# Optimization experiments

Hardware: AMD Instinct MI355X
Metric: run time of the kernel (lower is better)

The kernel has to match this reference:

```python
import jax, jax.numpy as jnp
import numpy as np

B, T, D, H = 128, 512, 1024, 1024


def setup_inputs() -> dict:
    key = jax.random.key(0)
    ks = jax.random.split(key, 9)
    s = 1.0 / np.sqrt(D + H)
    return {
        "inputs": jax.random.normal(ks[0], (B, T, D), dtype=jnp.float32),
        "Wf": jax.random.normal(ks[1], (D + H, H), dtype=jnp.float32) * s,
        "bf": jax.random.normal(ks[2], (H,), dtype=jnp.float32) * s,
        "Wi": jax.random.normal(ks[3], (D + H, H), dtype=jnp.float32) * s,
        "bi": jax.random.normal(ks[4], (H,), dtype=jnp.float32) * s,
        "Wo": jax.random.normal(ks[5], (D + H, H), dtype=jnp.float32) * s,
        "bo": jax.random.normal(ks[6], (H,), dtype=jnp.float32) * s,
        "Wc": jax.random.normal(ks[7], (D + H, H), dtype=jnp.float32) * s,
        "bc": jax.random.normal(ks[8], (H,), dtype=jnp.float32) * s,
    }


def reference(inputs, Wf, bf, Wi, bi, Wo, bo, Wc, bc):
    # inputs: [B, T, D]; gates computed from concat(x_t, h_t) @ W + b.
    # Fuse the 4 gate Linears into one GEMM (same math, single contraction).
    batch = inputs.shape[0]
    hid = Wf.shape[1]
    W = jnp.concatenate([Wf, Wi, Wo, Wc], axis=1)          # [D+H, 4H]
    b = jnp.concatenate([bf, bi, bo, bc])                   # [4H]

    def step(carry, x_t):
        h, c = carry
        z = jnp.concatenate([x_t, h], axis=1) @ W + b        # [B, 4H]
        f, i, o, g = jnp.split(z, 4, axis=1)
        f = jax.nn.sigmoid(f)
        i = jax.nn.sigmoid(i)
        o = jax.nn.sigmoid(o)
        g = jnp.tanh(g)
        c = f * c + i * g
        h = o * jnp.tanh(c)
        return (h, c), h

    h0 = jnp.zeros((batch, hid), dtype=inputs.dtype)
    c0 = jnp.zeros((batch, hid), dtype=inputs.dtype)
    _, hs = jax.lax.scan(step, (h0, c0), jnp.swapaxes(inputs, 0, 1))  # hs: [T, B, H]
    # Original prepends each new hidden state -> outputs are in REVERSE time order.
    return jnp.flip(jnp.swapaxes(hs, 0, 1), axis=1)          # [B, T, H]
```

## Files before the change

### kernel.cpp

```cpp
#include <hip/hip_runtime.h>
#include <hip/hip_bf16.h>

#define Bb 128
#define Tt 512
#define Dd 1024
#define Hh 1024
#define KD 2048
#define CCH 32
#define NCHUNK (Tt / CCH)
#define NBLK 256

typedef __attribute__((ext_vector_type(4))) float f32x4;
typedef __attribute__((ext_vector_type(8))) short s16x8;
typedef __attribute__((address_space(1))) const void gcvoid;
typedef __attribute__((address_space(3))) void lvoid;

__device__ __forceinline__ unsigned short f2bf(float f) {
    union { float f; unsigned u; } v;
    v.f = f;
    unsigned r = v.u + 0x7fffu + ((v.u >> 16) & 1u);
    return (unsigned short)(r >> 16);
}

__device__ __forceinline__ s16x8 cvt8(const float* src) {
    f32x4 a = *reinterpret_cast<const f32x4*>(src);
    f32x4 b = *reinterpret_cast<const f32x4*>(src + 4);
    s16x8 v;
    v[0] = (short)f2bf(a[0]); v[1] = (short)f2bf(a[1]);
    v[2] = (short)f2bf(a[2]); v[3] = (short)f2bf(a[3]);
    v[4] = (short)f2bf(b[0]); v[5] = (short)f2bf(b[1]);
    v[6] = (short)f2bf(b[2]); v[7] = (short)f2bf(b[3]);
    return v;
}

__device__ __forceinline__ float sigf(float x)      { return 1.f / (1.f + __expf(-x)); }
__device__ __forceinline__ float tanhfast(float x)  { return 1.f - 2.f / (1.f + __expf(2.f * x)); }

__device__ __forceinline__ void cload16(s16x8* dst, const unsigned short* p) {
    asm volatile("global_load_dwordx4 %0, %1, off sc1"
                 : "=v"(*dst) : "v"(p) : "memory");
}
__device__ __forceinline__ void cstore2(unsigned short* p, unsigned v) {
    asm volatile("global_store_short %0, %1, off sc1" :: "v"(p), "v"(v) : "memory");
}

__device__ __forceinline__ void gbar(unsigned* cntA, unsigned* cntB,
                                     unsigned* flag, int t, int bid) {
    asm volatile("s_waitcnt vmcnt(0)" ::: "memory");
    __syncthreads();
    if (threadIdx.x == 0) {
        unsigned* ca = cntA + ((size_t)t * 8 + (bid & 7)) * 32;
        unsigned o = __hip_atomic_fetch_add(ca, 1u, __ATOMIC_RELAXED, __HIP_MEMORY_SCOPE_AGENT);
        if (o == 31u) {
            unsigned* cb = cntB + (size_t)t * 32;
            unsigned o2 = __hip_atomic_fetch_add(cb, 1u, __ATOMIC_RELAXED, __HIP_MEMORY_SCOPE_AGENT);
            if (o2 == 7u)
                __hip_atomic_store(flag + t, 1u, __ATOMIC_RELAXED, __HIP_MEMORY_SCOPE_AGENT);
        }
        while (__hip_atomic_load(flag + t, __ATOMIC_RELAXED, __HIP_MEMORY_SCOPE_AGENT) == 0u)
            __builtin_amdgcn_s_sleep(1);
    }
    __syncthreads();
}

__global__ __launch_bounds__(256) void zx_gemm(
    const float* __restrict__ X, const unsigned short* __restrict__ Wr,
    const float* __restrict__ bre, float* __restrict__ Zxc, int t0)
{
    __shared__ __align__(16) unsigned short ALds[2][128 * 64];
    __shared__ __align__(16) unsigned short BLds[2][128 * 64];

    const int tid = threadIdx.x, lane = tid & 63, wv = tid >> 6;
    const int wr = wv >> 1, wc = wv & 1;
    const int m0 = (blockIdx.x >> 5) * 128, n0 = (blockIdx.x & 31) * 128;

    f32x4 acc[4][4];
#pragma unroll
    for (int i = 0; i < 4; ++i)
#pragma unroll
        for (int jn = 0; jn < 4; ++jn) acc[i][jn] = 0.f;

    auto stage = [&](int buf, int ki) {
        const int k0 = ki * 64;
#pragma unroll
        for (int i = 0; i < 4; ++i) {
            int slot = i * 256 + tid;
            int r = slot >> 3, cp = slot & 7;
            int c = cp ^ (r & 7);
            int m = m0 + r, b = m >> 5, tc = m & 31;
            const float* src = X + ((size_t)b * Tt + t0 + tc) * Dd + k0 + c * 8;
            *reinterpret_cast<s16x8*>(&ALds[buf][slot * 8]) = cvt8(src);
        }
#pragma unroll
        for (int i = 0; i < 4; ++i) {
            int slot = i * 256 + tid;
            int r = slot >> 3, cp = slot & 7;
            int c = cp ^ (r & 7);
            const unsigned short* src = Wr + (size_t)(n0 + r) * KD + k0 + c * 8;
            *reinterpret_cast<s16x8*>(&BLds[buf][slot * 8]) =
                *reinterpret_cast<const s16x8*>(src);
        }
    };

    auto compute = [&](int buf) {
#pragma unroll
        for (int ks = 0; ks < 2; ++ks) {
            int ck = ks * 4 + (lane >> 4);
            s16x8 af[4], bf8[4];
#pragma unroll
            for (int m = 0; m < 4; ++m) {
                int ra = wr * 64 + m * 16 + (lane & 15);
                af[m] = *reinterpret_cast<const s16x8*>(&ALds[buf][ra * 64 + (ck ^ (ra & 7)) * 8]);
            }
#pragma unroll
            for (int n = 0; n < 4; ++n) {
                int rb = wc * 64 + n * 16 + (lane & 15);
                bf8[n] = *reinterpret_cast<const s16x8*>(&BLds[buf][rb * 64 + (ck ^ (rb & 7)) * 8]);
            }
#pragma unroll
            for (int m = 0; m < 4; ++m)
#pragma unroll
                for (int n = 0; n < 4; ++n)
                    acc[m][n] = __builtin_amdgcn_mfma_f32_16x16x32_bf16(af[m], bf8[n], acc[m][n], 0, 0, 0);
        }
    };

    stage(0, 0);
#pragma unroll 1
    for (int ki = 0; ki < 16; ++ki) {
        __syncthreads();
        if (ki + 1 < 16) stage((ki + 1) & 1, ki + 1);
        compute(ki & 1);
    }

#pragma unroll
    for (int ni = 0; ni < 4; ++ni) {
        int gcol = n0 + wc * 64 + ni * 16 + (lane & 15);
        float bias = bre[gcol];
        int gg = gcol >> 5, nn = gcol & 31;
        int zcol = gg * 32 + (nn & 7) * 4 + (nn >> 3);
#pragma unroll
        for (int mi = 0; mi < 4; ++mi) {
            int rbase = m0 + wr * 64 + mi * 16 + (lane >> 4) * 4;
#pragma unroll
            for (int r = 0; r < 4; ++r)
                Zxc[(size_t)(rbase + r) * 4096 + zcol] = acc[mi][ni][r] + bias;
        }
    }
}

__global__ __launch_bounds__(256) void lstm_chunk(
    const unsigned short* __restrict__ Wr,
    const float* __restrict__ Zxc,
    unsigned short* __restrict__ hbuf,
    float* __restrict__ cbuf,
    float* __restrict__ out,
    unsigned* __restrict__ cntA,
    unsigned* __restrict__ cntB,
    unsigned* __restrict__ flag,
    int t0)
{
    __shared__ __align__(16) unsigned short Bl[32 * 1024];

    const int tid = threadIdx.x, lane = tid & 63, w = tid >> 6;
    const int bid = blockIdx.x;
    const int g = bid >> 1, mh = bid & 1;

#pragma unroll
    for (int i = 0; i < 16; ++i) {
        int q = (w * 16 + i) * 64 + lane;
        int n = q >> 7, cp = q & 127;
        int cs = (cp & ~7) | ((cp ^ n) & 7);
        const unsigned short* src = Wr + (size_t)(g * 32 + n) * KD + Dd + cs * 8;
        __builtin_amdgcn_global_load_lds((gcvoid*)src,
            (lvoid*)&Bl[(w * 16 + i) * 512], 16, 0, 0);
    }
    asm volatile("s_waitcnt vmcnt(0)" ::: "memory");
    __syncthreads();

    const int r0 = mh * 64 + w * 16 + (lane & 15);
    const int nlo = lane & 15;
    const unsigned short* b0p = &Bl[nlo * 1024];
    const int jj = lane & 7, j = g * 8 + jj;
    const bool hi = (lane & 8) != 0;
    const int rowb = mh * 64 + w * 16 + (lane >> 4) * 4;

    f32x4 creg;
#pragma unroll
    for (int r = 0; r < 4; ++r)
        creg[r] = cbuf[(size_t)(rowb + r) * Hh + j];

    f32x4 zx[4];
#pragma unroll
    for (int r = 0; r < 4; ++r)
        zx[r] = *reinterpret_cast<const f32x4*>(
            Zxc + ((size_t)(rowb + r) * CCH + 0) * 4096 + j * 4);

#pragma unroll 1
    for (int tt = 0; tt < CCH; ++tt) {
        const int t = t0 + tt;
        const unsigned short* hin = hbuf + (size_t)(t & 1) * (Bb * Hh);
        unsigned short* houtp = hbuf + (size_t)((t + 1) & 1) * (Bb * Hh);
        const unsigned short* arow = hin + (size_t)r0 * Hh + (lane >> 4) * 8;

        f32x4 acc0 = 0.f, acc1 = 0.f;

        s16x8 afb[2][8];
#pragma unroll
        for (int i = 0; i < 8; ++i)
            cload16(&afb[0][i], arow + i * 32);

#pragma unroll
        for (int b = 0; b < 4; ++b) {
            if (b < 3) {
#pragma unroll
                for (int i = 0; i < 8; ++i)
                    cload16(&afb[(b + 1) & 1][i], arow + ((b + 1) * 8 + i) * 32);
                asm volatile("s_waitcnt vmcnt(8)" ::: "memory");
            } else {
                asm volatile("s_waitcnt vmcnt(0)" ::: "memory");
            }
            __builtin_amdgcn_sched_barrier(0);
#pragma unroll
            for (int i = 0; i < 8; ++i) {
                int ki = b * 8 + i;
                int ck = ki * 4 + (lane >> 4);
                int p = (ck & ~7) | ((ck ^ nlo) & 7);
                s16x8 b0 = *reinterpret_cast<const s16x8*>(b0p + p * 8);
                s16x8 b1 = *reinterpret_cast<const s16x8*>(b0p + 16 * 1024 + p * 8);
                acc0 = __builtin_amdgcn_mfma_f32_16x16x32_bf16(afb[b & 1][i], b0, acc0, 0, 0, 0);
                acc1 = __builtin_amdgcn_mfma_f32_16x16x32_bf16(afb[b & 1][i], b1, acc1, 0, 0, 0);
            }
        }

        f32x4 y0, y1;
#pragma unroll
        for (int r = 0; r < 4; ++r) {
            y0[r] = __shfl_xor(acc0[r], 8, 64);
            y1[r] = __shfl_xor(acc1[r], 8, 64);
        }

        f32x4 zxn[4];
        if (tt + 1 < CCH) {
#pragma unroll
            for (int r = 0; r < 4; ++r)
                zxn[r] = *reinterpret_cast<const f32x4*>(
                    Zxc + ((size_t)(rowb + r) * CCH + (tt + 1)) * 4096 + j * 4);
        }

#pragma unroll
        for (int r = 0; r < 4; ++r) {
            float vf = hi ? y0[r] : acc0[r];
            float vi = hi ? acc0[r] : y0[r];
            float vo = hi ? y1[r] : acc1[r];
            float vg = hi ? acc1[r] : y1[r];
            float zf = vf + zx[r][0], zi = vi + zx[r][1];
            float zo = vo + zx[r][2], zc = vg + zx[r][3];
            float fg = sigf(zf), ig = sigf(zi), og = sigf(zo), gv = tanhfast(zc);
            float cnew = fg * creg[r] + ig * gv;
            creg[r] = cnew;
            float hn = og * tanhfast(cnew);
            int row = rowb + r;
            cstore2(houtp + (size_t)row * Hh + j, (unsigned)f2bf(hn));
            out[((size_t)row * Tt + (Tt - 1 - t)) * Hh + j] = hn;
        }
#pragma unroll
        for (int r = 0; r < 4; ++r) zx[r] = zxn[r];

        if (tt + 1 < CCH) gbar(cntA, cntB, flag, t, bid);
    }

#pragma unroll
    for (int r = 0; r < 4; ++r)
        cbuf[(size_t)(rowb + r) * Hh + j] = creg[r];
}

__global__ __launch_bounds__(256) void conv_w(
    const float* __restrict__ Wf, const float* __restrict__ Wi,
    const float* __restrict__ Wo, const float* __restrict__ Wc,
    unsigned short* __restrict__ Wr)
{
    __shared__ float sm[64 * 65];
    const int tid = threadIdx.x;
    const int bid = blockIdx.x;
    const int gate = bid & 3;
    const int rest = bid >> 2;
    const int k0 = (rest & 31) * 64;
    const int c0 = (rest >> 5) * 64;
    const float* Wg = (gate == 0) ? Wf : (gate == 1) ? Wi : (gate == 2) ? Wo : Wc;

#pragma unroll
    for (int it = 0; it < 16; ++it) {
        int kl = it * 4 + (tid >> 6), cl = tid & 63;
        sm[kl * 65 + cl] = Wg[(size_t)(k0 + kl) * Hh + c0 + cl];
    }
    __syncthreads();
#pragma unroll
    for (int it = 0; it < 16; ++it) {
        int nl = it * 4 + (tid >> 6), kl = tid & 63;
        int col = c0 + nl;
        int n = (col >> 3) * 32 + gate * 8 + (col & 7);
        Wr[(size_t)n * KD + k0 + kl] = f2bf(sm[kl * 65 + nl]);
    }
}

#define NBAR_U32 (512 * 8 * 32 + 512 * 32 + 512)

__global__ void init_all(unsigned short* __restrict__ hbuf, float* __restrict__ cbuf,
                         unsigned* __restrict__ bars, float* __restrict__ bre,
                         const float* __restrict__ bF, const float* __restrict__ bI,
                         const float* __restrict__ bO, const float* __restrict__ bC) {
    int i = blockIdx.x * 256 + threadIdx.x;
    if (i < 2 * Bb * Hh) hbuf[i] = 0;
    if (i < Bb * Hh) cbuf[i] = 0.f;
    if (i < NBAR_U32) bars[i] = 0u;
    if (i < 4096) {
        int gate = (i >> 3) & 3, g = i >> 5, jjv = i & 7;
        int col = g * 8 + jjv;
        const float* bg = (gate == 0) ? bF : (gate == 1) ? bI : (gate == 2) ? bO : bC;
        bre[i] = bg[col];
    }
}

__global__ __launch_bounds__(256) void lstm_step(
    const float* __restrict__ X, const unsigned short* __restrict__ Wr,
    const float* __restrict__ bre,
    const unsigned short* __restrict__ hin, unsigned short* __restrict__ hout,
    float* __restrict__ cbuf, float* __restrict__ out, int t)
{
    __shared__ __align__(16) unsigned short Alds[2][64 * 64];
    __shared__ __align__(16) unsigned short Blds[2][32 * 64];
    __shared__ float zlds[64 * 33];

    const int tid = threadIdx.x, lane = tid & 63, w = tid >> 6;
    const int g = blockIdx.x >> 1, mh = blockIdx.x & 1;

    f32x4 acc[2];
    acc[0] = 0.f; acc[1] = 0.f;

    auto stageA = [&](int buf, int ki) {
        const int k0 = ki * 64;
#pragma unroll
        for (int i = 0; i < 2; ++i) {
            int slot = tid + 256 * i;
            int r = slot >> 3, cp = slot & 7;
            int c = cp ^ (r & 7);
            int k = k0 + c * 8;
            s16x8 v;
            if (k < Dd) {
                v = cvt8(X + ((size_t)(mh * 64 + r) * Tt + t) * Dd + k);
            } else {
                v = *reinterpret_cast<const s16x8*>(hin + (size_t)(mh * 64 + r) * Hh + (k - Dd));
            }
            *reinterpret_cast<s16x8*>(&Alds[buf][slot * 8]) = v;
        }
    };
    auto stageB = [&](int buf, int ki) {
        int n = tid >> 3, cp = tid & 7;
        int c = cp ^ (n & 7);
        const unsigned short* src = Wr + (size_t)(g * 32 + n) * KD + ki * 64 + c * 8;
        *reinterpret_cast<s16x8*>(&Blds[buf][tid * 8]) = *reinterpret_cast<const s16x8*>(src);
    };
    auto compute = [&](int buf) {
#pragma unroll
        for (int ks = 0; ks < 2; ++ks) {
            int ra = w * 16 + (lane & 15);
            int cha = (ks * 4 + (lane >> 4)) ^ (ra & 7);
            s16x8 af = *reinterpret_cast<const s16x8*>(&Alds[buf][ra * 64 + cha * 8]);
#pragma unroll
            for (int nt = 0; nt < 2; ++nt) {
                int n = nt * 16 + (lane & 15);
                int chb = (ks * 4 + (lane >> 4)) ^ (n & 7);
                s16x8 bf8 = *reinterpret_cast<const s16x8*>(&Blds[buf][n * 64 + chb * 8]);
                acc[nt] = __builtin_amdgcn_mfma_f32_16x16x32_bf16(af, bf8, acc[nt], 0, 0, 0);
            }
        }
    };

    stageA(0, 0); stageB(0, 0);
#pragma unroll 1
    for (int ki = 0; ki < 32; ++ki) {
        __syncthreads();
        if (ki + 1 < 32) { stageA((ki + 1) & 1, ki + 1); stageB((ki + 1) & 1, ki + 1); }
        compute(ki & 1);
    }

    {
        int rbase = w * 16 + (lane >> 4) * 4;
#pragma unroll
        for (int nt = 0; nt < 2; ++nt) {
            int col = nt * 16 + (lane & 15);
#pragma unroll
            for (int r = 0; r < 4; ++r)
                zlds[(rbase + r) * 33 + col] = acc[nt][r];
        }
    }
    __syncthreads();

#pragma unroll
    for (int it = 0; it < 2; ++it) {
        int idx = tid + it * 256;
        int row = idx >> 3, jj = idx & 7;
        int jx = g * 8 + jj;
        int grow = mh * 64 + row;
        float zf = zlds[row * 33 + jj]      + bre[g * 32 + jj];
        float zi = zlds[row * 33 + 8 + jj]  + bre[g * 32 + 8 + jj];
        float zo = zlds[row * 33 + 16 + jj] + bre[g * 32 + 16 + jj];
        float zc = zlds[row * 33 + 24 + jj] + bre[g * 32 + 24 + jj];
        float fg = sigf(zf), ig = sigf(zi), og = sigf(zo), gv = tanhfast(zc);
        float cold = cbuf[(size_t)grow * Hh + jx];
        float cnew = fg * cold + ig * gv;
        cbuf[(size_t)grow * Hh + jx] = cnew;
        float hn = og * tanhfast(cnew);
        hout[(size_t)grow * Hh + jx] = f2bf(hn);
        out[((size_t)grow * Tt + (Tt - 1 - t)) * Hh + jx] = hn;
    }
}

extern "C" void kernel_launch(void* const* d_in, const int* in_sizes, int n_in,
                              void* d_out, int out_size, void* d_ws, size_t ws_size,
                              hipStream_t stream) {
    (void)in_sizes; (void)n_in; (void)out_size;
    const float* X  = (const float*)d_in[0];
    const float* Wf = (const float*)d_in[1];
    const float* bF = (const float*)d_in[2];
    const float* Wi = (const float*)d_in[3];
    const float* bI = (const float*)d_in[4];
    const float* Wo = (const float*)d_in[5];
    const float* bO = (const float*)d_in[6];
    const float* Wc = (const float*)d_in[7];
    const float* bC = (const float*)d_in[8];
    float* out = (float*)d_out;

    char* ws = (char*)d_ws;
    size_t off = 0;
    auto carve = [&](size_t sz) { char* p = ws + off; off = (off + sz + 255) & ~(size_t)255; return p; };
    unsigned short* Wr   = (unsigned short*)carve((size_t)4096 * KD * 2);
    float*          bre  = (float*)carve(4096 * 4);
    unsigned short* hbuf = (unsigned short*)carve((size_t)2 * Bb * Hh * 2);
    float*          cbuf = (float*)carve((size_t)Bb * Hh * 4);
    unsigned*       bars = (unsigned*)carve((size_t)NBAR_U32 * 4);
    float*          Zxc  = (float*)carve((size_t)4096 * 4096 * 4);
    const size_t need = off;

    unsigned* cntA = bars;
    unsigned* cntB = bars + 512 * 8 * 32;
    unsigned* flag = bars + 512 * 8 * 32 + 512 * 32;

    conv_w<<<2048, 256, 0, stream>>>(Wf, Wi, Wo, Wc, Wr);
    init_all<<<1024, 256, 0, stream>>>(hbuf, cbuf, bars, bre, bF, bI, bO, bC);

    if (ws_size >= need) {
        const unsigned short* Wr_c = Wr;
        const float* Zxc_c = Zxc;
        for (int c = 0; c < NCHUNK; ++c) {
            int t0 = c * CCH;
            zx_gemm<<<1024, 256, 0, stream>>>(X, Wr, bre, Zxc, t0);
            void* args[] = {(void*)&Wr_c, (void*)&Zxc_c, (void*)&hbuf, (void*)&cbuf,
                            (void*)&out, (void*)&cntA, (void*)&cntB, (void*)&flag, (void*)&t0};
            hipLaunchCooperativeKernel((void*)lstm_chunk, dim3(NBLK), dim3(256), args, 0, stream);
        }
    } else {
        for (int t = 0; t < Tt; ++t) {
            const unsigned short* hin = hbuf + (size_t)(t & 1) * Bb * Hh;
            unsigned short*      houtp = hbuf + (size_t)((t + 1) & 1) * Bb * Hh;
            lstm_step<<<256, 256, 0, stream>>>(X, Wr, bre, hin, houtp, cbuf, out, t);
        }
    }
}
```

Measured before the change: 5.402 ms.

## Halve recurrent blocks to 128, widen per-block hidden slice, use flag-array grid barrier

The recurrent chunk kernel now runs 128 cooperative blocks instead of 256. Each block owns 16 hidden units across all 4 gates and keeps a 128KB LDS slice of the recurrent weights, so all four gate accumulators sit in registers and the cross-lane shuffles go away. The weight, bias and Zx column layouts are remapped to match. The two-level atomic counter barrier is replaced by per-block flag stores that one wavefront polls with vector loads, which is meant to cut barrier latency per timestep. In exchange each block does twice the MFMA work per step, so fewer CUs are active, and it depends on 128KB of LDS per block fitting.

Result: slower. 6.139 ms (+13.6%).

```diff
diff --git a/kernel.cpp b/kernel.cpp
--- a/kernel.cpp
+++ b/kernel.cpp
@@ -8,10 +8,11 @@
 #define KD 2048
 #define CCH 32
 #define NCHUNK (Tt / CCH)
-#define NBLK 256
+#define NBLK 128
 
 typedef __attribute__((ext_vector_type(4))) float f32x4;
 typedef __attribute__((ext_vector_type(8))) short s16x8;
+typedef __attribute__((ext_vector_type(4))) unsigned u32x4;
 typedef __attribute__((address_space(1))) const void gcvoid;
 typedef __attribute__((address_space(3))) void lvoid;
 
@@ -44,21 +45,23 @@
     asm volatile("global_store_short %0, %1, off sc1" :: "v"(p), "v"(v) : "memory");
 }
 
-__device__ __forceinline__ void gbar(unsigned* cntA, unsigned* cntB,
-                                     unsigned* flag, int t, int bid) {
+__device__ __forceinline__ void gbar(unsigned* flags, int t, int bid) {
     asm volatile("s_waitcnt vmcnt(0)" ::: "memory");
     __syncthreads();
-    if (threadIdx.x == 0) {
-        unsigned* ca = cntA + ((size_t)t * 8 + (bid & 7)) * 32;
-        unsigned o = __hip_atomic_fetch_add(ca, 1u, __ATOMIC_RELAXED, __HIP_MEMORY_SCOPE_AGENT);
-        if (o == 31u) {
-            unsigned* cb = cntB + (size_t)t * 32;
-            unsigned o2 = __hip_atomic_fetch_add(cb, 1u, __ATOMIC_RELAXED, __HIP_MEMORY_SCOPE_AGENT);
-            if (o2 == 7u)
-                __hip_atomic_store(flag + t, 1u, __ATOMIC_RELAXED, __HIP_MEMORY_SCOPE_AGENT);
-        }
-        while (__hip_atomic_load(flag + t, __ATOMIC_RELAXED, __HIP_MEMORY_SCOPE_AGENT) == 0u)
+    if (threadIdx.x < 64) {
+        unsigned* base = flags + (size_t)t * NBLK;
+        if (threadIdx.x == 0)
+            asm volatile("global_store_dword %0, %1, off sc1"
+                         :: "v"(base + bid), "v"(1u) : "memory");
+        const unsigned* sp = base + (threadIdx.x & 31) * 4;
+        for (;;) {
+            u32x4 f;
+            asm volatile("global_load_dwordx4 %0, %1, off sc1"
+                         : "=v"(f) : "v"(sp) : "memory");
+            asm volatile("s_waitcnt vmcnt(0)" ::: "memory");
+            if (__all((f[0] & f[1] & f[2] & f[3]) != 0u)) break;
             __builtin_amdgcn_s_sleep(1);
+        }
     }
     __syncthreads();
 }
@@ -137,8 +140,8 @@
     for (int ni = 0; ni < 4; ++ni) {
         int gcol = n0 + wc * 64 + ni * 16 + (lane & 15);
         float bias = bre[gcol];
-        int gg = gcol >> 5, nn = gcol & 31;
-        int zcol = gg * 32 + (nn & 7) * 4 + (nn >> 3);
+        int g = gcol >> 6, rem = gcol & 63, gate = rem >> 4, jj = rem & 15;
+        int zcol = (g * 16 + jj) * 4 + gate;
 #pragma unroll
         for (int mi = 0; mi < 4; ++mi) {
             int rbase = m0 + wr * 64 + mi * 16 + (lane >> 4) * 4;
@@ -155,34 +158,31 @@
     unsigned short* __restrict__ hbuf,
     float* __restrict__ cbuf,
     float* __restrict__ out,
-    unsigned* __restrict__ cntA,
-    unsigned* __restrict__ cntB,
-    unsigned* __restrict__ flag,
+    unsigned* __restrict__ flags,
     int t0)
 {
-    __shared__ __align__(16) unsigned short Bl[32 * 1024];
+    __shared__ __align__(16) unsigned short Bl[64 * 1024];
 
     const int tid = threadIdx.x, lane = tid & 63, w = tid >> 6;
     const int bid = blockIdx.x;
     const int g = bid >> 1, mh = bid & 1;
 
 #pragma unroll
-    for (int i = 0; i < 16; ++i) {
-        int q = (w * 16 + i) * 64 + lane;
+    for (int i = 0; i < 32; ++i) {
+        int q = (w * 32 + i) * 64 + lane;
         int n = q >> 7, cp = q & 127;
         int cs = (cp & ~7) | ((cp ^ n) & 7);
-        const unsigned short* src = Wr + (size_t)(g * 32 + n) * KD + Dd + cs * 8;
+        const unsigned short* src = Wr + (size_t)(g * 64 + n) * KD + Dd + cs * 8;
         __builtin_amdgcn_global_load_lds((gcvoid*)src,
-            (lvoid*)&Bl[(w * 16 + i) * 512], 16, 0, 0);
+            (lvoid*)&Bl[(w * 32 + i) * 512], 16, 0, 0);
     }
     asm volatile("s_waitcnt vmcnt(0)" ::: "memory");
     __syncthreads();
 
-    const int r0 = mh * 64 + w * 16 + (lane & 15);
     const int nlo = lane & 15;
+    const int r0 = mh * 64 + w * 16 + nlo;
     const unsigned short* b0p = &Bl[nlo * 1024];
-    const int jj = lane & 7, j = g * 8 + jj;
-    const bool hi = (lane & 8) != 0;
+    const int j = g * 16 + nlo;
     const int rowb = mh * 64 + w * 16 + (lane >> 4) * 4;
 
     f32x4 creg;
@@ -203,7 +203,9 @@
         unsigned short* houtp = hbuf + (size_t)((t + 1) & 1) * (Bb * Hh);
         const unsigned short* arow = hin + (size_t)r0 * Hh + (lane >> 4) * 8;
 
-        f32x4 acc0 = 0.f, acc1 = 0.f;
+        f32x4 acc[4];
+#pragma unroll
+        for (int n = 0; n < 4; ++n) acc[n] = 0.f;
 
         s16x8 afb[2][8];
 #pragma unroll
@@ -226,18 +228,12 @@
                 int ki = b * 8 + i;
                 int ck = ki * 4 + (lane >> 4);
                 int p = (ck & ~7) | ((ck ^ nlo) & 7);
-                s16x8 b0 = *reinterpret_cast<const s16x8*>(b0p + p * 8);
-                s16x8 b1 = *reinterpret_cast<const s16x8*>(b0p + 16 * 1024 + p * 8);
-                acc0 = __builtin_amdgcn_mfma_f32_16x16x32_bf16(afb[b & 1][i], b0, acc0, 0, 0, 0);
-                acc1 = __builtin_amdgcn_mfma_f32_16x16x32_bf16(afb[b & 1][i], b1, acc1, 0, 0, 0);
-            }
-        }
-
-        f32x4 y0, y1;
-#pragma unroll
-        for (int r = 0; r < 4; ++r) {
-            y0[r] = __shfl_xor(acc0[r], 8, 64);
-            y1[r] = __shfl_xor(acc1[r], 8, 64);
+#pragma unroll
+                for (int n = 0; n < 4; ++n) {
+                    s16x8 bf8 = *reinterpret_cast<const s16x8*>(b0p + n * 16384 + p * 8);
+                    acc[n] = __builtin_amdgcn_mfma_f32_16x16x32_bf16(afb[b & 1][i], bf8, acc[n], 0, 0, 0);
+                }
+            }
         }
 
         f32x4 zxn[4];
@@ -250,12 +246,10 @@
 
 #pragma unroll
         for (int r = 0; r < 4; ++r) {
-            float vf = hi ? y0[r] : acc0[r];
-            float vi = hi ? acc0[r] : y0[r];
-            float vo = hi ? y1[r] : acc1[r];
-            float vg = hi ? acc1[r] : y1[r];
-            float zf = vf + zx[r][0], zi = vi + zx[r][1];
-            float zo = vo + zx[r][2], zc = vg + zx[r][3];
+            float zf = acc[0][r] + zx[r][0];
+            float zi = acc[1][r] + zx[r][1];
+            float zo = acc[2][r] + zx[r][2];
+            float zc = acc[3][r] + zx[r][3];
             float fg = sigf(zf), ig = sigf(zi), og = sigf(zo), gv = tanhfast(zc);
             float cnew = fg * creg[r] + ig * gv;
             creg[r] = cnew;
@@ -267,7 +261,7 @@
 #pragma unroll
         for (int r = 0; r < 4; ++r) zx[r] = zxn[r];
 
-        if (tt + 1 < CCH) gbar(cntA, cntB, flag, t, bid);
+        if (tt + 1 < CCH) gbar(flags, t, bid);
     }
 
 #pragma unroll
@@ -299,24 +293,55 @@
     for (int it = 0; it < 16; ++it) {
         int nl = it * 4 + (tid >> 6), kl = tid & 63;
         int col = c0 + nl;
+        int n = (col >> 4) * 64 + gate * 16 + (col & 15);
+        Wr[(size_t)n * KD + k0 + kl] = f2bf(sm[kl * 65 + nl]);
+    }
+}
+
+__global__ __launch_bounds__(256) void conv_w_old(
+    const float* __restrict__ Wf, const float* __restrict__ Wi,
+    const float* __restrict__ Wo, const float* __restrict__ Wc,
+    unsigned short* __restrict__ Wr)
+{
+    __shared__ float sm[64 * 65];
+    const int tid = threadIdx.x;
+    const int bid = blockIdx.x;
+    const int gate = bid & 3;
+    const int rest = bid >> 2;
+    const int k0 = (rest & 31) * 64;
+    const int c0 = (rest >> 5) * 64;
+    const float* Wg = (gate == 0) ? Wf : (gate == 1) ? Wi : (gate == 2) ? Wo : Wc;
+
+#pragma unroll
+    for (int it = 0; it < 16; ++it) {
+        int kl = it * 4 + (tid >> 6), cl = tid & 63;
+        sm[kl * 65 + cl] = Wg[(size_t)(k0 + kl) * Hh + c0 + cl];
+    }
+    __syncthreads();
+#pragma unroll
+    for (int it = 0; it < 16; ++it) {
+        int nl = it * 4 + (tid >> 6), kl = tid & 63;
+        int col = c0 + nl;
         int n = (col >> 3) * 32 + gate * 8 + (col & 7);
         Wr[(size_t)n * KD + k0 + kl] = f2bf(sm[kl * 65 + nl]);
     }
 }
 
-#define NBAR_U32 (512 * 8 * 32 + 512 * 32 + 512)
+#define NBAR_U32 (512 * NBLK)
 
 __global__ void init_all(unsigned short* __restrict__ hbuf, float* __restrict__ cbuf,
                          unsigned* __restrict__ bars, float* __restrict__ bre,
                          const float* __restrict__ bF, const float* __restrict__ bI,
-                         const float* __restrict__ bO, const float* __restrict__ bC) {
+                         const float* __restrict__ bO, const float* __restrict__ bC,
+                         int newmap) {
     int i = blockIdx.x * 256 + threadIdx.x;
     if (i < 2 * Bb * Hh) hbuf[i] = 0;
     if (i < Bb * Hh) cbuf[i] = 0.f;
     if (i < NBAR_U32) bars[i] = 0u;
     if (i < 4096) {
-        int gate = (i >> 3) & 3, g = i >> 5, jjv = i & 7;
-        int col = g * 8 + jjv;
+        int gate, col;
+        if (newmap) { gate = (i >> 4) & 3; col = (i >> 6) * 16 + (i & 15); }
+        else        { gate = (i >> 3) & 3; col = (i >> 5) * 8  + (i & 7); }
         const float* bg = (gate == 0) ? bF : (gate == 1) ? bI : (gate == 2) ? bO : bC;
         bre[i] = bg[col];
     }
@@ -443,21 +468,21 @@
     float*          Zxc  = (float*)carve((size_t)4096 * 4096 * 4);
     const size_t need = off;
 
-    unsigned* cntA = bars;
-    unsigned* cntB = bars + 512 * 8 * 32;
-    unsigned* flag = bars + 512 * 8 * 32 + 512 * 32;
-
-    conv_w<<<2048, 256, 0, stream>>>(Wf, Wi, Wo, Wc, Wr);
-    init_all<<<1024, 256, 0, stream>>>(hbuf, cbuf, bars, bre, bF, bI, bO, bC);
-
-    if (ws_size >= need) {
+    const bool main_path = (ws_size >= need);
+
+    if (main_path) conv_w<<<2048, 256, 0, stream>>>(Wf, Wi, Wo, Wc, Wr);
+    else           conv_w_old<<<2048, 256, 0, stream>>>(Wf, Wi, Wo, Wc, Wr);
+    init_all<<<1024, 256, 0, stream>>>(hbuf, cbuf, bars, bre, bF, bI, bO, bC,
+                                       main_path ? 1 : 0);
+
+    if (main_path) {
         const unsigned short* Wr_c = Wr;
         const float* Zxc_c = Zxc;
         for (int c = 0; c < NCHUNK; ++c) {
             int t0 = c * CCH;
             zx_gemm<<<1024, 256, 0, stream>>>(X, Wr, bre, Zxc, t0);
             void* args[] = {(void*)&Wr_c, (void*)&Zxc_c, (void*)&hbuf, (void*)&cbuf,
-                            (void*)&out, (void*)&cntA, (void*)&cntB, (void*)&flag, (void*)&t0};
+                            (void*)&out, (void*)&bars, (void*)&t0};
             hipLaunchCooperativeKernel((void*)lstm_chunk, dim3(NBLK), dim3(256), args, 0, stream);
         }
     } else {
```
